# Optimization experiments

Hardware: AMD Instinct MI355X
Metric: run time of the kernel (lower is better)

## Reference

```python
import jax, jax.numpy as jnp
import numpy as np

N_SAMPLES_DEPTHS = [64, 32, 16]
DEPTH_RES_LEVELS = [2, 2, 2]
NV = 3
IMG_H = IMG_W = 512
VOL = 128


def trilinear_lookup(vol, pts):
    """Trilinear sample of vol[D,H,W] at pts[...,3] in [-1,1] (x->W, y->H, z->D).
    Matches F.grid_sample(mode='bilinear', padding_mode='border', align_corners=True)."""
    D, H, W = vol.shape
    x = jnp.clip((pts[..., 0] + 1.0) * 0.5 * (W - 1), 0.0, W - 1.0)
    y = jnp.clip((pts[..., 1] + 1.0) * 0.5 * (H - 1), 0.0, H - 1.0)
    z = jnp.clip((pts[..., 2] + 1.0) * 0.5 * (D - 1), 0.0, D - 1.0)
    x0f = jnp.floor(x); y0f = jnp.floor(y); z0f = jnp.floor(z)
    wx = x - x0f; wy = y - y0f; wz = z - z0f
    x0 = x0f.astype(jnp.int32); y0 = y0f.astype(jnp.int32); z0 = z0f.astype(jnp.int32)
    x1 = jnp.minimum(x0 + 1, W - 1)
    y1 = jnp.minimum(y0 + 1, H - 1)
    z1 = jnp.minimum(z0 + 1, D - 1)
    c000 = vol[z0, y0, x0]; c001 = vol[z0, y0, x1]
    c010 = vol[z0, y1, x0]; c011 = vol[z0, y1, x1]
    c100 = vol[z1, y0, x0]; c101 = vol[z1, y0, x1]
    c110 = vol[z1, y1, x0]; c111 = vol[z1, y1, x1]
    c00 = c000 * (1 - wx) + c001 * wx
    c01 = c010 * (1 - wx) + c011 * wx
    c10 = c100 * (1 - wx) + c101 * wx
    c11 = c110 * (1 - wx) + c111 * wx
    c0 = c00 * (1 - wy) + c01 * wy
    c1 = c10 * (1 - wy) + c11 * wy
    return c0 * (1 - wz) + c1 * wz


def _make_c2w(angle):
    c, s = np.cos(angle), np.sin(angle)
    m = np.eye(4, dtype=np.float32)
    m[:3, :3] = np.array([[c, 0, s], [0, 1, 0], [-s, 0, c]], np.float32)
    m[:3, 3] = np.array([0.3 * np.sin(angle), 0.0, -1.5], np.float32)
    return m


def setup_inputs() -> dict:
    key = jax.random.key(0)
    k_img, k_vol = jax.random.split(key)
    imgs = jax.random.normal(k_img, (NV, 3, IMG_H, IMG_W), dtype=jnp.float32)
    f = 400.0
    intr = np.array([[f, 0.0, IMG_W / 2], [0.0, f, IMG_H / 2], [0.0, 0.0, 1.0]], np.float32)
    intrs = jnp.asarray(np.stack([intr] * NV))
    c2ws = jnp.asarray(np.stack([_make_c2w(a) for a in (0.0, 0.15, -0.15)]))
    near_fars = jnp.tile(jnp.array([[0.5, 3.0]], jnp.float32), (NV, 1))
    density_volume = jax.random.normal(k_vol, (VOL, VOL, VOL), dtype=jnp.float32)
    return {"imgs": imgs, "intrs": intrs, "c2ws": c2ws, "near_fars": near_fars,
            "density_volume": density_volume, "stage_idx": 0}


def reference(imgs, intrs, c2ws, near_fars, density_volume, stage_idx):
    img_h, img_w = imgs.shape[-2:]
    res = DEPTH_RES_LEVELS[stage_idx]
    h, w = img_h // res, img_w // res
    n_s = N_SAMPLES_DEPTHS[stage_idx]

    # pixel grid at reduced resolution (matches torch.meshgrid 'ij')
    ty = jnp.linspace(0.0, img_h - 1.0, h)
    tx = jnp.linspace(0.0, img_w - 1.0, w)
    py, px = jnp.meshgrid(ty, tx, indexing='ij')
    pixels = jnp.stack([px.reshape(-1), py.reshape(-1), jnp.ones(h * w, jnp.float32)], -1)  # [N,3]
    t_lin = jnp.linspace(0.0, 1.0, n_s)  # [S]

    def render_view(c2w, intr, near_far):
        cam = pixels @ jnp.linalg.inv(intr).T                      # [N,3]
        rays_d = cam / jnp.linalg.norm(cam, axis=-1, keepdims=True)
        rays_d = rays_d @ c2w[:3, :3].T                            # world-space dirs
        z_vals = near_far[0] + (near_far[1] - near_far[0]) * t_lin  # [S] (single stage: already sorted)
        pts = c2w[None, None, :3, 3] + rays_d[:, None, :] * z_vals[None, :, None]  # [N,S,3]
        outside = jax.lax.stop_gradient((jnp.linalg.norm(pts, axis=-1) > 1.0).astype(pts.dtype))  # [N,S]
        density = trilinear_lookup(density_volume, pts)            # [N,S]
        weights = jax.nn.softmax(density, axis=-1)
        cam_rays_d = rays_d @ jnp.linalg.inv(c2w[:3, :3]).T        # back to camera frame
        render_z = jnp.sum(z_vals[None, :] * weights, axis=1)      # [N]
        render_depth = (render_z * cam_rays_d[:, 2]).reshape(h, w)
        occ_reg = density[:, :6].mean() + (density * outside).sum() / (outside.sum() + 1e-10)
        depth_full = jax.image.resize(render_depth, (img_h, img_w), method='bilinear')
        return depth_full, occ_reg

    depths, occs = jax.vmap(render_view)(c2ws, intrs, near_fars)
    # views other than src_idx=0 are rendered under no_grad in the original
    depths = jnp.concatenate([depths[:1], jax.lax.stop_gradient(depths[1:])], axis=0)
    occs = jnp.concatenate([occs[:1], jax.lax.stop_gradient(occs[1:])], axis=0)
    return depths, occs
```

## Files before the change

kernel.cpp:

```cpp
#include <hip/hip_runtime.h>
#include <hip/hip_fp16.h>
#include <math.h>

#define NVIEW 3
#define HLOW 256
#define WLOW 256
#define NPIX (HLOW * WLOW)
#define NS 64
#define VOLN 128
#define IMGH 512
#define IMGW 512
#define BLK 256
#define BLOCKS_PER_VIEW (NPIX / BLK)
#define NVOX (VOLN * VOLN * VOLN)
#define UPS2_BLOCKS ((NVIEW * IMGH * IMGW / 2) / BLK)
#define NXCD 8
#define MARCH_BLOCKS (NVIEW * BLOCKS_PER_VIEW)
#define CHUNK (MARCH_BLOCKS / NXCD)

#define LOG2E     1.4426950408889634f
#define INV_LOG2E 0.6931471805599453f

typedef _Float16 h2 __attribute__((ext_vector_type(2)));

struct Ray {
    float ax0, axs, ay0, ays, az0, azs;
    float sLo, sHi;
    float z0, zstep, ncz;
};

__device__ __forceinline__ Ray ray_setup(
    int view, int row, int col,
    const float* __restrict__ intrs, const float* __restrict__ c2ws,
    const float* __restrict__ nf)
{
    const float px = 511.0f * (float)col * (1.0f / 255.0f);
    const float py = 511.0f * (float)row * (1.0f / 255.0f);

    const float* K = intrs + view * 9;
    const float a = K[0], b = K[1], c = K[2];
    const float d = K[3], e = K[4], f = K[5];
    const float g = K[6], h = K[7], i9 = K[8];
    const float det = a * (e * i9 - f * h) - b * (d * i9 - f * g) + c * (d * h - e * g);
    const float id = 1.0f / det;
    const float m00 = (e * i9 - f * h) * id, m01 = -(b * i9 - c * h) * id, m02 = (b * f - c * e) * id;
    const float m10 = -(d * i9 - f * g) * id, m11 = (a * i9 - c * g) * id, m12 = -(a * f - c * d) * id;
    const float m20 = (d * h - e * g) * id, m21 = -(a * h - b * g) * id, m22 = (a * e - b * d) * id;

    const float cx = m00 * px + m01 * py + m02;
    const float cy = m10 * px + m11 * py + m12;
    const float cz = m20 * px + m21 * py + m22;
    const float inr = rsqrtf(cx * cx + cy * cy + cz * cz);
    const float ncz = cz * inr;

    const float ncx = cx * inr, ncy = cy * inr;
    const float* M = c2ws + view * 16;
    const float dx = M[0] * ncx + M[1] * ncy + M[2] * ncz;
    const float dy = M[4] * ncx + M[5] * ncy + M[6] * ncz;
    const float dz = M[8] * ncx + M[9] * ncy + M[10] * ncz;
    const float tx = M[3], ty = M[7], tz = M[11];

    const float z0 = nf[view * 2 + 0];
    const float zstep = (nf[view * 2 + 1] - z0) * (1.0f / 63.0f);

    Ray r;
    const float gx0 = (tx + 1.0f) * 63.5f, gxs = dx * 63.5f;
    const float gy0 = (ty + 1.0f) * 63.5f, gys = dy * 63.5f;
    const float gz0 = (tz + 1.0f) * 63.5f, gzs = dz * 63.5f;
    r.ax0 = fmaf(gxs, z0, gx0); r.axs = gxs * zstep;
    r.ay0 = fmaf(gys, z0, gy0); r.ays = gys * zstep;
    r.az0 = fmaf(gzs, z0, gz0); r.azs = gzs * zstep;

    const float bq = tx * dx + ty * dy + tz * dz;
    const float cq = tx * tx + ty * ty + tz * tz;
    const float disc = bq * bq - (cq - 1.0f);
    if (disc >= 0.0f) {
        const float rt = sqrtf(disc);
        const float inv = 1.0f / zstep;
        r.sLo = (-bq - rt - z0) * inv;
        r.sHi = (-bq + rt - z0) * inv;
    } else {
        r.sLo = 3.4e38f;
        r.sHi = 0.0f;
    }

    r.z0 = z0;
    r.zstep = zstep;
    r.ncz = ncz;
    return r;
}

__global__ __launch_bounds__(BLK) void build_pack8_kernel(
    const float* __restrict__ vol, uint2* __restrict__ P)
{
    const int id = blockIdx.x * BLK + threadIdx.x;
    const int x = id & 127;
    const int y = (id >> 7) & 127;
    const int z = id >> 14;
    const int yp = min(y + 1, 127);
    const int zp = min(z + 1, 127);

    const float v00 = vol[(z  * VOLN + y ) * VOLN + x];
    const float v01 = vol[(z  * VOLN + yp) * VOLN + x];
    const float v10 = vol[(zp * VOLN + y ) * VOLN + x];
    const float v11 = vol[(zp * VOLN + yp) * VOLN + x];

    const __half2 w0 = __floats2half2_rn(v00 * LOG2E, v01 * LOG2E);
    const __half2 w1 = __floats2half2_rn(v10 * LOG2E, v11 * LOG2E);
    uint2 o;
    o.x = *reinterpret_cast<const unsigned*>(&w0);
    o.y = *reinterpret_cast<const unsigned*>(&w1);
    P[id] = o;
}

__global__ __launch_bounds__(BLK) void raymarch_pack8_kernel(
    const float* __restrict__ intrs, const float* __restrict__ c2ws,
    const float* __restrict__ nf, const char* __restrict__ Fb,
    float* __restrict__ depth_low, float* __restrict__ partials)
{
    const int wg  = blockIdx.x;
    const int swz = (wg & (NXCD - 1)) * CHUNK + (wg >> 3);
    const int view = swz >> 8;
    const int row  = swz & 255;
    const int t    = threadIdx.x;

    const Ray r = ray_setup(view, row, t, intrs, c2ws, nf);

    const float ilo = ceilf(fmaxf(r.sLo, 0.0f));
    const float ihi = floorf(fminf(r.sHi, 63.0f));
    const float cnt = 64.0f - fmaxf(0.0f, ihi - ilo + 1.0f);

    float lsum = 0.0f, sacc = 0.0f, d6 = 0.0f, dout = 0.0f;

    h2 fx2[2][8], fyw[2][8];
    float fzs[2][8];
    uint4 q[2][8];

#define ADDR_BATCH(BK, SB)                                                    \
    {                                                                         \
        unsigned offs[8];                                                     \
        _Pragma("unroll")                                                     \
        for (int i = 0; i < 8; ++i) {                                         \
            const float sf = (float)((SB) + i);                               \
            float gx = fmaf(r.axs, sf, r.ax0);                                \
            float gy = fmaf(r.ays, sf, r.ay0);                                \
            float gz = fmaf(r.azs, sf, r.az0);                                \
            gx = fminf(fmaxf(gx, 0.0f), 126.9995f);                           \
            gy = fminf(fmaxf(gy, 0.0f), 126.9995f);                           \
            gz = fminf(fmaxf(gz, 0.0f), 126.9995f);                           \
            const float xbf = floorf(gx);                                     \
            const float ybf = floorf(gy);                                     \
            const float zbf = floorf(gz);                                     \
            const float fx = gx - xbf;                                        \
            const float fy = gy - ybf;                                        \
            fzs[BK][i] = gz - zbf;                                            \
            fx2[BK][i] = (h2){(_Float16)fx, (_Float16)fx};                    \
            fyw[BK][i] = (h2){(_Float16)(1.0f - fy), (_Float16)fy};           \
            offs[i] = (unsigned)fmaf(zbf, 16384.0f, fmaf(ybf, 128.0f, xbf));  \
        }                                                                     \
        _Pragma("unroll")                                                     \
        for (int i = 0; i < 8; ++i)                                           \
            q[BK][i] = *reinterpret_cast<const uint4*>(Fb + (size_t)offs[i] * 8); \
    }

#define CONSUME_BATCH(BK, SB)                                                 \
    _Pragma("unroll")                                                         \
    for (int i = 0; i < 8; ++i) {                                             \
        const float sf = (float)((SB) + i);                                   \
        const h2 w0 = __builtin_bit_cast(h2, q[BK][i].x);                     \
        const h2 w1 = __builtin_bit_cast(h2, q[BK][i].y);                     \
        const h2 w2 = __builtin_bit_cast(h2, q[BK][i].z);                     \
        const h2 w3 = __builtin_bit_cast(h2, q[BK][i].w);                     \
        const h2 cx0 = fx2[BK][i] * (w2 - w0) + w0;          \
        const h2 cx1 = fx2[BK][i] * (w3 - w1) + w1;          \
        const float c0 = __builtin_amdgcn_fdot2(cx0, fyw[BK][i], 0.0f, false);\
        const float c1 = __builtin_amdgcn_fdot2(cx1, fyw[BK][i], 0.0f, false);\
        const float dens = fmaf(fzs[BK][i], c1 - c0, c0);      \
        const float w = exp2f(dens);                             \
        lsum += w;                                                            \
        sacc = fmaf(sf, w, sacc);                                             \
        if ((SB) == 0 && i < 6) d6 += dens;                                   \
        const bool o = (sf < r.sLo) || (sf > r.sHi);                          \
        dout += o ? dens : 0.0f;                                              \
    }

    ADDR_BATCH(0, 0)
    #pragma unroll
    for (int b = 0; b < 8; ++b) {
        if (b < 7) {
            if (b & 1) { ADDR_BATCH(0, (b + 1) * 8) }
            else       { ADDR_BATCH(1, (b + 1) * 8) }
        }
        if (b & 1) { CONSUME_BATCH(1, b * 8) }
        else       { CONSUME_BATCH(0, b * 8) }
    }
#undef ADDR_BATCH
#undef CONSUME_BATCH

    depth_low[view * NPIX + row * WLOW + t] =
        fmaf(r.zstep, sacc / lsum, r.z0) * r.ncz;

    __shared__ float s0[BLK], s1[BLK], s2[BLK];
    s0[t] = d6; s1[t] = dout; s2[t] = cnt;
    __syncthreads();
    for (int off = BLK / 2; off > 0; off >>= 1) {
        if (t < off) {
            s0[t] += s0[t + off];
            s1[t] += s1[t + off];
            s2[t] += s2[t + off];
        }
        __syncthreads();
    }
    if (t == 0) {
        partials[swz * 3 + 0] = s0[0] * INV_LOG2E;
        partials[swz * 3 + 1] = s1[0] * INV_LOG2E;
        partials[swz * 3 + 2] = s2[0];
    }
}

__global__ __launch_bounds__(BLK) void raymarch_f32_kernel(
    const float* __restrict__ intrs, const float* __restrict__ c2ws,
    const float* __restrict__ nf, const float* __restrict__ vol,
    float* __restrict__ depth_low, float* __restrict__ partials)
{
    const int view = blockIdx.x >> 8;
    const int row  = blockIdx.x & 255;
    const int t    = threadIdx.x;

    const Ray r = ray_setup(view, row, t, intrs, c2ws, nf);

    const float ilo = ceilf(fmaxf(r.sLo, 0.0f));
    const float ihi = floorf(fminf(r.sHi, 63.0f));
    const float cnt = 64.0f - fmaxf(0.0f, ihi - ilo + 1.0f);

    float lsum = 0.0f, sacc = 0.0f, d6 = 0.0f, dout = 0.0f;

    #pragma unroll 16
    for (int s = 0; s < NS; ++s) {
        const float sf = (float)s;
        float gx = fmaf(r.axs, sf, r.ax0);
        float gy = fmaf(r.ays, sf, r.ay0);
        float gz = fmaf(r.azs, sf, r.az0);
        gx = fminf(fmaxf(gx, 0.0f), 126.9995f);
        gy = fminf(fmaxf(gy, 0.0f), 126.9995f);
        gz = fminf(fmaxf(gz, 0.0f), 126.9995f);
        const float xbf = floorf(gx);
        const float ybf = floorf(gy);
        const float zbf = floorf(gz);
        const float fx = gx - xbf, fy = gy - ybf, fz = gz - zbf;
        const unsigned off = (unsigned)fmaf(zbf, 16384.0f, fmaf(ybf, 128.0f, xbf));

        const float* p0 = vol + off;
        const float2 v00 = *reinterpret_cast<const float2*>(p0);
        const float2 v01 = *reinterpret_cast<const float2*>(p0 + VOLN);
        const float2 v10 = *reinterpret_cast<const float2*>(p0 + VOLN * VOLN);
        const float2 v11 = *reinterpret_cast<const float2*>(p0 + VOLN * VOLN + VOLN);

        const float c00 = fmaf(fx, v00.y - v00.x, v00.x);
        const float c01 = fmaf(fx, v01.y - v01.x, v01.x);
        const float c10 = fmaf(fx, v10.y - v10.x, v10.x);
        const float c11 = fmaf(fx, v11.y - v11.x, v11.x);
        const float c0 = fmaf(fy, c01 - c00, c00);
        const float c1 = fmaf(fy, c11 - c10, c10);
        const float dens = fmaf(fz, c1 - c0, c0);

        const float w = __expf(dens);
        lsum += w;
        sacc = fmaf(sf, w, sacc);

        if (s < 6) d6 += dens;
        const bool o = (sf < r.sLo) || (sf > r.sHi);
        dout += o ? dens : 0.0f;
    }

    depth_low[view * NPIX + row * WLOW + t] =
        fmaf(r.zstep, sacc / lsum, r.z0) * r.ncz;

    __shared__ float s0[BLK], s1[BLK], s2[BLK];
    s0[t] = d6; s1[t] = dout; s2[t] = cnt;
    __syncthreads();
    for (int off = BLK / 2; off > 0; off >>= 1) {
        if (t < off) {
            s0[t] += s0[t + off];
            s1[t] += s1[t + off];
            s2[t] += s2[t + off];
        }
        __syncthreads();
    }
    if (t == 0) {
        partials[blockIdx.x * 3 + 0] = s0[0];
        partials[blockIdx.x * 3 + 1] = s1[0];
        partials[blockIdx.x * 3 + 2] = s2[0];
    }
}

__global__ __launch_bounds__(BLK) void epilogue_kernel(
    const float* __restrict__ low, const float* __restrict__ partials,
    float* __restrict__ out)
{
    if (blockIdx.x >= UPS2_BLOCKS) {
        const int view = blockIdx.x - UPS2_BLOCKS;
        const int t = threadIdx.x;
        __shared__ float s0[BLK], s1[BLK], s2[BLK];
        const int bi = view * BLOCKS_PER_VIEW + t;
        s0[t] = partials[bi * 3 + 0];
        s1[t] = partials[bi * 3 + 1];
        s2[t] = partials[bi * 3 + 2];
        __syncthreads();
        for (int off = BLK / 2; off > 0; off >>= 1) {
            if (t < off) {
                s0[t] += s0[t + off];
                s1[t] += s1[t + off];
                s2[t] += s2[t + off];
            }
            __syncthreads();
        }
        if (t == 0) {
            out[NVIEW * IMGH * IMGW + view] =
                s0[0] * (1.0f / (float)(NPIX * 6)) + s1[0] / (s2[0] + 1e-10f);
        }
        return;
    }

    const int idx2 = blockIdx.x * BLK + threadIdx.x;
    const int view = idx2 / (IMGH * IMGW / 2);
    const int rem  = idx2 - view * (IMGH * IMGW / 2);
    const int rr = rem >> 8;
    const int cp = rem & 255;
    const int cc0 = cp * 2;

    const float sy = (float)rr * 0.5f - 0.25f;
    const float y0f = floorf(sy);
    const float wy = sy - y0f;
    const int y0 = (int)y0f;
    const int y0c = max(y0, 0), y1c = min(y0 + 1, HLOW - 1);
    const float* src = low + view * NPIX;
    const float* r0 = src + y0c * WLOW;
    const float* r1 = src + y1c * WLOW;

    float2 res;
    {
        const float sx = (float)cc0 * 0.5f - 0.25f;
        const float x0f = floorf(sx);
        const float wx = sx - x0f;
        const int x0 = (int)x0f;
        const int x0c = max(x0, 0), x1c = min(x0 + 1, WLOW - 1);
        const float top = r0[x0c] * (1.0f - wx) + r0[x1c] * wx;
        const float bot = r1[x0c] * (1.0f - wx) + r1[x1c] * wx;
        res.x = top * (1.0f - wy) + bot * wy;
    }
    {
        const int cc1 = cc0 + 1;
        const float sx = (float)cc1 * 0.5f - 0.25f;
        const float x0f = floorf(sx);
        const float wx = sx - x0f;
        const int x0 = (int)x0f;
        const int x0c = max(x0, 0), x1c = min(x0 + 1, WLOW - 1);
        const float top = r0[x0c] * (1.0f - wx) + r0[x1c] * wx;
        const float bot = r1[x0c] * (1.0f - wx) + r1[x1c] * wx;
        res.y = top * (1.0f - wy) + bot * wy;
    }
    *reinterpret_cast<float2*>(out + view * (IMGH * IMGW) + rr * IMGW + cc0) = res;
}

extern "C" void kernel_launch(void* const* d_in, const int* in_sizes, int n_in,
                              void* d_out, int out_size, void* d_ws, size_t ws_size,
                              hipStream_t stream) {
    const float* intrs = (const float*)d_in[1];
    const float* c2ws  = (const float*)d_in[2];
    const float* nf    = (const float*)d_in[3];
    const float* vol   = (const float*)d_in[4];
    float* out = (float*)d_out;

    const size_t pack_bytes  = (size_t)NVOX * 8 + 16;
    const size_t depth_bytes = (size_t)NVIEW * NPIX * 4;
    const size_t part_bytes  = (size_t)NVIEW * BLOCKS_PER_VIEW * 3 * 4;
    char* ws = (char*)d_ws;

    float* depth_low;
    float* partials;

    if (ws_size >= pack_bytes + depth_bytes + part_bytes) {
        uint2* P = (uint2*)ws;
        depth_low = (float*)(ws + pack_bytes);
        partials  = depth_low + NVIEW * NPIX;
        build_pack8_kernel<<<NVOX / BLK, BLK, 0, stream>>>(vol, P);
        raymarch_pack8_kernel<<<MARCH_BLOCKS, BLK, 0, stream>>>(
            intrs, c2ws, nf, (const char*)ws, depth_low, partials);
    } else {
        depth_low = (float*)ws;
        partials  = depth_low + NVIEW * NPIX;
        raymarch_f32_kernel<<<MARCH_BLOCKS, BLK, 0, stream>>>(
            intrs, c2ws, nf, vol, depth_low, partials);
    }

    epilogue_kernel<<<UPS2_BLOCKS + NVIEW, BLK, 0, stream>>>(depth_low, partials, out);
}
```

Before: 34.72 us.

## Split each ray's samples across two threads with interleaved parity

Each ray is now handled by a pair of threads, each taking alternating samples (even or odd), and partial softmax sums are combined with a lane shuffle. Blocks cover 128 rays, which doubles the march grid, and the epilogue reduction now loops over a variable number of partials per view. The aim is more threads in flight and a shorter serial dependency chain per thread, which hides gather latency better. The cost is redundant ray setup per pair and a larger partials reduction.

```diff
diff --git a/kernel.cpp b/kernel.cpp
--- a/kernel.cpp
+++ b/kernel.cpp
@@ -11,12 +11,17 @@
 #define IMGH 512
 #define IMGW 512
 #define BLK 256
-#define BLOCKS_PER_VIEW (NPIX / BLK)
 #define NVOX (VOLN * VOLN * VOLN)
 #define UPS2_BLOCKS ((NVIEW * IMGH * IMGW / 2) / BLK)
 #define NXCD 8
-#define MARCH_BLOCKS (NVIEW * BLOCKS_PER_VIEW)
+
+#define RAYS_PER_BLOCK 128
+#define BPV_MARCH (NPIX / RAYS_PER_BLOCK)
+#define MARCH_BLOCKS (NVIEW * BPV_MARCH)
 #define CHUNK (MARCH_BLOCKS / NXCD)
+
+#define BPV_F32 (NPIX / BLK)
+#define F32_BLOCKS (NVIEW * BPV_F32)
 
 #define LOG2E     1.4426950408889634f
 #define INV_LOG2E 0.6931471805599453f
@@ -120,15 +125,21 @@
 {
     const int wg  = blockIdx.x;
     const int swz = (wg & (NXCD - 1)) * CHUNK + (wg >> 3);
-    const int view = swz >> 8;
-    const int row  = swz & 255;
+    const int view = swz / BPV_MARCH;
+    const int rb   = swz - view * BPV_MARCH;
     const int t    = threadIdx.x;
-
-    const Ray r = ray_setup(view, row, t, intrs, c2ws, nf);
+    const int rloc = t >> 1;
+    const int par  = t & 1;
+    const int ray  = rb * RAYS_PER_BLOCK + rloc;
+    const int row  = ray >> 8;
+    const int col  = ray & 255;
+
+    const Ray r = ray_setup(view, row, col, intrs, c2ws, nf);
 
     const float ilo = ceilf(fmaxf(r.sLo, 0.0f));
     const float ihi = floorf(fminf(r.sHi, 63.0f));
     const float cnt = 64.0f - fmaxf(0.0f, ihi - ilo + 1.0f);
+    const float parf = (float)par;
 
     float lsum = 0.0f, sacc = 0.0f, d6 = 0.0f, dout = 0.0f;
 
@@ -141,7 +152,7 @@
         unsigned offs[8];                                                     \
         _Pragma("unroll")                                                     \
         for (int i = 0; i < 8; ++i) {                                         \
-            const float sf = (float)((SB) + i);                               \
+            const float sf = (float)((SB) + 2 * i) + parf;                    \
             float gx = fmaf(r.axs, sf, r.ax0);                                \
             float gy = fmaf(r.ays, sf, r.ay0);                                \
             float gz = fmaf(r.azs, sf, r.az0);                                \
@@ -166,7 +177,7 @@
 #define CONSUME_BATCH(BK, SB)                                                 \
     _Pragma("unroll")                                                         \
     for (int i = 0; i < 8; ++i) {                                             \
-        const float sf = (float)((SB) + i);                                   \
+        const float sf = (float)((SB) + 2 * i) + parf;                        \
         const h2 w0 = __builtin_bit_cast(h2, q[BK][i].x);                     \
         const h2 w1 = __builtin_bit_cast(h2, q[BK][i].y);                     \
         const h2 w2 = __builtin_bit_cast(h2, q[BK][i].z);                     \
@@ -179,29 +190,30 @@
         const float w = exp2f(dens);                             \
         lsum += w;                                                            \
         sacc = fmaf(sf, w, sacc);                                             \
-        if ((SB) == 0 && i < 6) d6 += dens;                                   \
+        if ((SB) == 0 && i < 3) d6 += dens;           \
         const bool o = (sf < r.sLo) || (sf > r.sHi);                          \
         dout += o ? dens : 0.0f;                                              \
     }
 
     ADDR_BATCH(0, 0)
-    #pragma unroll
-    for (int b = 0; b < 8; ++b) {
-        if (b < 7) {
-            if (b & 1) { ADDR_BATCH(0, (b + 1) * 8) }
-            else       { ADDR_BATCH(1, (b + 1) * 8) }
-        }
-        if (b & 1) { CONSUME_BATCH(1, b * 8) }
-        else       { CONSUME_BATCH(0, b * 8) }
-    }
+    ADDR_BATCH(1, 16)
+    CONSUME_BATCH(0, 0)
+    ADDR_BATCH(0, 32)
+    CONSUME_BATCH(1, 16)
+    ADDR_BATCH(1, 48)
+    CONSUME_BATCH(0, 32)
+    CONSUME_BATCH(1, 48)
 #undef ADDR_BATCH
 #undef CONSUME_BATCH
 
-    depth_low[view * NPIX + row * WLOW + t] =
-        fmaf(r.zstep, sacc / lsum, r.z0) * r.ncz;
+    lsum += __shfl_xor(lsum, 1);
+    sacc += __shfl_xor(sacc, 1);
+    if (par == 0)
+        depth_low[view * NPIX + ray] =
+            fmaf(r.zstep, sacc / lsum, r.z0) * r.ncz;
 
     __shared__ float s0[BLK], s1[BLK], s2[BLK];
-    s0[t] = d6; s1[t] = dout; s2[t] = cnt;
+    s0[t] = d6; s1[t] = dout; s2[t] = par ? 0.0f : cnt;
     __syncthreads();
     for (int off = BLK / 2; off > 0; off >>= 1) {
         if (t < off) {
@@ -296,16 +308,20 @@
 
 __global__ __launch_bounds__(BLK) void epilogue_kernel(
     const float* __restrict__ low, const float* __restrict__ partials,
-    float* __restrict__ out)
+    float* __restrict__ out, int nppv)
 {
     if (blockIdx.x >= UPS2_BLOCKS) {
         const int view = blockIdx.x - UPS2_BLOCKS;
         const int t = threadIdx.x;
         __shared__ float s0[BLK], s1[BLK], s2[BLK];
-        const int bi = view * BLOCKS_PER_VIEW + t;
-        s0[t] = partials[bi * 3 + 0];
-        s1[t] = partials[bi * 3 + 1];
-        s2[t] = partials[bi * 3 + 2];
+        float a0 = 0.0f, a1 = 0.0f, a2 = 0.0f;
+        for (int k = t; k < nppv; k += BLK) {
+            const int bi = view * nppv + k;
+            a0 += partials[bi * 3 + 0];
+            a1 += partials[bi * 3 + 1];
+            a2 += partials[bi * 3 + 2];
+        }
+        s0[t] = a0; s1[t] = a1; s2[t] = a2;
         __syncthreads();
         for (int off = BLK / 2; off > 0; off >>= 1) {
             if (t < off) {
@@ -374,7 +390,7 @@
 
     const size_t pack_bytes  = (size_t)NVOX * 8 + 16;
     const size_t depth_bytes = (size_t)NVIEW * NPIX * 4;
-    const size_t part_bytes  = (size_t)NVIEW * BLOCKS_PER_VIEW * 3 * 4;
+    const size_t part_bytes  = (size_t)MARCH_BLOCKS * 3 * 4;
     char* ws = (char*)d_ws;
 
     float* depth_low;
@@ -387,12 +403,14 @@
         build_pack8_kernel<<<NVOX / BLK, BLK, 0, stream>>>(vol, P);
         raymarch_pack8_kernel<<<MARCH_BLOCKS, BLK, 0, stream>>>(
             intrs, c2ws, nf, (const char*)ws, depth_low, partials);
+        epilogue_kernel<<<UPS2_BLOCKS + NVIEW, BLK, 0, stream>>>(
+            depth_low, partials, out, BPV_MARCH);
     } else {
         depth_low = (float*)ws;
         partials  = depth_low + NVIEW * NPIX;
-        raymarch_f32_kernel<<<MARCH_BLOCKS, BLK, 0, stream>>>(
+        raymarch_f32_kernel<<<F32_BLOCKS, BLK, 0, stream>>>(
             intrs, c2ws, nf, vol, depth_low, partials);
-    }
-
-    epilogue_kernel<<<UPS2_BLOCKS + NVIEW, BLK, 0, stream>>>(depth_low, partials, out);
-}
+        epilogue_kernel<<<UPS2_BLOCKS + NVIEW, BLK, 0, stream>>>(
+            depth_low, partials, out, BPV_F32);
+    }
+}
```

New measurement: 56.09 us. 1.62x slower.
